# Optimization experiments

Hardware: AMD Instinct MI355X
Metric: run time of the kernel (lower is better)

## Reference

```python
import jax, jax.numpy as jnp
import numpy as np

POOL = 100      # e_pool_size
PLEN = 8        # e_p_length
EMB = 768       # emb_d
KEYD = 768      # key_dim
B = 256
SOFT_T = 1.0    # prompt_param[-1]
VQ_COEF = 0.4
COMIT_COEF = 0.1
E_LAYERS = (0, 1, 2, 3, 4)


def setup_inputs() -> dict:
    key = jax.random.key(0)
    k1, k2, k3, k4 = jax.random.split(key, 4)
    x_querry = jax.random.normal(k1, (B, KEYD), dtype=jnp.float32)
    x_block = jax.random.normal(k2, (B, 197, EMB), dtype=jnp.float32)
    # learned params: nn.init.uniform_ -> U[0,1)
    K = jax.random.uniform(k3, (POOL, KEYD), dtype=jnp.float32)
    p = jax.random.uniform(k4, (POOL, PLEN, EMB), dtype=jnp.float32)
    return {"x_querry": x_querry, "l": 0, "x_block": x_block, "K": K, "p": p}


def reference(x_querry, l, x_block, K, p):
    if l not in E_LAYERS:
        return (None, jnp.float32(0.0), x_block)
    # cosine-sim attention over prompt keys
    n_K = K / jnp.maximum(jnp.linalg.norm(K, axis=1, keepdims=True), 1e-12)
    cos_sim = jnp.einsum('bd,kd->bk', x_querry, n_K)
    alpha = jax.nn.softmax(cos_sim / SOFT_T, axis=1)
    p_a = jnp.einsum('bk,kld->bld', alpha, p)  # [B, L, D]
    # squared L2 distance to each pool entry via dot products (no BxKxLxD tensor)
    pa_sq = jnp.sum(p_a * p_a, axis=(1, 2))            # [B]
    pp_sq = jnp.sum(p * p, axis=(1, 2))                # [K]
    cross = jnp.einsum('bld,kld->bk', p_a, p)          # [B, K]
    dist = pa_sq[:, None] - 2.0 * cross + pp_sq[None, :]
    idxmin = jnp.argmin(dist, axis=1)                  # [B]
    quantized = p[idxmin]                              # [B, L, D]
    e_latent_loss = jnp.mean((p_a - jax.lax.stop_gradient(quantized)) ** 2)
    q_latent_loss = jnp.mean((quantized - jax.lax.stop_gradient(p_a)) ** 2)
    # straight-through estimator
    P_ = p_a + jax.lax.stop_gradient(quantized - p_a)
    i = PLEN // 2
    Ek = P_[:, :i, :]
    Ev = P_[:, i:, :]
    loss = VQ_COEF * e_latent_loss + COMIT_COEF * q_latent_loss
    return (Ek, Ev, loss, x_block)
```

## Files before the change

kernel.cpp:

```cpp
#include <hip/hip_runtime.h>

#define POOL 100
#define PLEN 8
#define EMB 768
#define KEYD 768
#define BATCH 256
#define LD (PLEN*EMB)
#define EK_FLOATS (BATCH*4*EMB)
#define XB_FLOATS (BATCH*197*EMB)
#define LOSS_OFF (2*EK_FLOATS)
#define XB_OFF (LOSS_OFF+1)
#define NGT 325
#define NCOS (BATCH*25)
#define N4 9689087
#define TILE 2048
#define NTILES 4731

typedef float v4f __attribute__((ext_vector_type(4)));
typedef v4f v4f_u __attribute__((aligned(4)));

__device__ __forceinline__ void gram_tile(const float* __restrict__ p,
                                          double* __restrict__ G, int t) {
    int gx = (int)((sqrt(8.0 * t + 1.0) - 1.0) * 0.5);
    while ((gx + 1) * (gx + 2) / 2 <= t) ++gx;
    while (gx * (gx + 1) / 2 > t) --gx;
    int gy = t - gx * (gx + 1) / 2;
    const v4f* P4 = (const v4f*)p;
    double acc[16];
    #pragma unroll
    for (int i = 0; i < 16; ++i) acc[i] = 0.0;
    #pragma unroll
    for (int ch = 0; ch < 6; ++ch) {
        int col = ch * 256 + threadIdx.x;
        v4f ay[4], ax[4];
        #pragma unroll
        for (int i = 0; i < 4; ++i) ay[i] = P4[(size_t)(4*gy + i) * 1536 + col];
        #pragma unroll
        for (int j = 0; j < 4; ++j) ax[j] = P4[(size_t)(4*gx + j) * 1536 + col];
        #pragma unroll
        for (int i = 0; i < 4; ++i)
            #pragma unroll
            for (int j = 0; j < 4; ++j)
                acc[i*4+j] += (double)ay[i][0]*ax[j][0] + (double)ay[i][1]*ax[j][1]
                            + (double)ay[i][2]*ax[j][2] + (double)ay[i][3]*ax[j][3];
    }
    #pragma unroll
    for (int i = 0; i < 16; ++i)
        for (int off = 32; off > 0; off >>= 1)
            acc[i] += __shfl_down(acc[i], off, 64);
    __shared__ double sg[4][16];
    int lane = threadIdx.x & 63, w = threadIdx.x >> 6;
    if (lane == 0) {
        #pragma unroll
        for (int i = 0; i < 16; ++i) sg[w][i] = acc[i];
    }
    __syncthreads();
    if (threadIdx.x < 16) {
        double v = sg[0][threadIdx.x] + sg[1][threadIdx.x]
                 + sg[2][threadIdx.x] + sg[3][threadIdx.x];
        int i = threadIdx.x >> 2, j = threadIdx.x & 3;
        int r = 4*gy + i, c = 4*gx + j;
        G[r * POOL + c] = v;
        G[c * POOL + r] = v;
    }
}

__device__ __forceinline__ void cos_unit(const float* __restrict__ xq,
                                         const float* __restrict__ K,
                                         double* __restrict__ cosm, int c) {
    int b = c / 25, kg = c % 25;
    int w = threadIdx.x >> 6, lane = threadIdx.x & 63;
    int k = kg * 4 + w;
    const v4f* kr = (const v4f*)(K + (size_t)k * KEYD);
    const v4f* xr = (const v4f*)(xq + (size_t)b * KEYD);
    double dot = 0.0, sq = 0.0;
    #pragma unroll
    for (int it = 0; it < 3; ++it) {
        v4f a = kr[it * 64 + lane];
        v4f x = xr[it * 64 + lane];
        dot += (double)a[0]*x[0] + (double)a[1]*x[1] + (double)a[2]*x[2] + (double)a[3]*x[3];
        sq  += (double)a[0]*a[0] + (double)a[1]*a[1] + (double)a[2]*a[2] + (double)a[3]*a[3];
    }
    for (int off = 32; off > 0; off >>= 1) {
        dot += __shfl_down(dot, off, 64);
        sq  += __shfl_down(sq,  off, 64);
    }
    if (lane == 0)
        cosm[(size_t)b * POOL + k] = dot / fmax(sqrt(sq), 1e-12);
}

__global__ void kprep(const float* __restrict__ p, const float* __restrict__ xq,
                      const float* __restrict__ K, const float* __restrict__ xb,
                      float* __restrict__ out, double* __restrict__ G,
                      double* __restrict__ cosm, double* __restrict__ lossAcc,
                      unsigned int* __restrict__ lossCnt) {
    int t = blockIdx.x;
    if (t == 0) {
        if (threadIdx.x == 64) { lossAcc[0] = 0.0; lossCnt[0] = 0u; }
        if (threadIdx.x == 65) {
            out[XB_OFF]     = xb[0];
            out[XB_OFF + 1] = xb[1];
            out[XB_OFF + 2] = xb[2];
            out[XB_OFF + XB_FLOATS - 1] = xb[XB_FLOATS - 1];
        }
    }
    if (t < NGT) gram_tile(p, G, t);
    else         cos_unit(xq, K, cosm, t - NGT);
}

__global__ void kmain(const double* __restrict__ cosm, const double* __restrict__ G,
                      const float* __restrict__ p, const float* __restrict__ xb,
                      float* __restrict__ out, double* __restrict__ lossAcc,
                      unsigned int* __restrict__ lossCnt) {
    if (blockIdx.x >= BATCH) {
        int tile = (int)(blockIdx.x - BATCH);
        const v4f* src4 = (const v4f*)xb;
        v4f* dst = (v4f*)(out + XB_OFF + 3);
        size_t base = (size_t)tile * TILE + threadIdx.x;
        int lane = threadIdx.x & 63;
        if (base + 7 * 256 < N4) {
            v4f v[8];
            #pragma unroll
            for (int k = 0; k < 8; ++k) v[k] = src4[base + (size_t)k * 256 + 1];
            float pw[8];
            #pragma unroll
            for (int k = 0; k < 8; ++k) pw[k] = __shfl_up(v[k][3], 1, 64);
            if (lane == 0) {
                #pragma unroll
                for (int k = 0; k < 8; ++k) pw[k] = xb[4 * (base + (size_t)k * 256) + 3];
            }
            #pragma unroll
            for (int k = 0; k < 8; ++k) {
                v4f o = {pw[k], v[k][0], v[k][1], v[k][2]};
                __builtin_nontemporal_store(o, &dst[base + (size_t)k * 256]);
            }
        } else {
            const v4f_u* srcu = (const v4f_u*)(xb + 3);
            #pragma unroll
            for (int k = 0; k < 8; ++k) {
                size_t j = base + (size_t)k * 256;
                if (j < N4) dst[j] = srcu[j];
            }
        }
        return;
    }
    int b = blockIdx.x;
    __shared__ double sa[POOL], sm[POOL];
    __shared__ double sred[4];
    __shared__ int sidx;
    int lane = threadIdx.x & 63, w = threadIdx.x >> 6;

    double cv = (threadIdx.x < POOL) ? cosm[(size_t)b * POOL + threadIdx.x] : -1.0e300;
    double m = cv;
    for (int off = 32; off > 0; off >>= 1) m = fmax(m, __shfl_down(m, off, 64));
    if (lane == 0) sred[w] = m;
    __syncthreads();
    m = fmax(fmax(sred[0], sred[1]), fmax(sred[2], sred[3]));
    __syncthreads();
    double e = (threadIdx.x < POOL) ? exp(cv - m) : 0.0;
    double ssum = e;
    for (int off = 32; off > 0; off >>= 1) ssum += __shfl_down(ssum, off, 64);
    if (lane == 0) sred[w] = ssum;
    __syncthreads();
    ssum = sred[0] + sred[1] + sred[2] + sred[3];
    __syncthreads();
    if (threadIdx.x < POOL) sa[threadIdx.x] = e / ssum;
    __syncthreads();
    double c = 0.0, paterm = 0.0;
    if (threadIdx.x < POOL) {
        #pragma unroll 4
        for (int k = 0; k < POOL; ++k)
            c += sa[k] * G[k * POOL + threadIdx.x];
        paterm = sa[threadIdx.x] * c;
        sm[threadIdx.x] = G[threadIdx.x * POOL + threadIdx.x] - 2.0 * c;
    }
    double pa = paterm;
    for (int off = 32; off > 0; off >>= 1) pa += __shfl_down(pa, off, 64);
    if (lane == 0) sred[w] = pa;
    __syncthreads();
    pa = sred[0] + sred[1] + sred[2] + sred[3];
    if (threadIdx.x == 0) {
        int best = 0; double bm = sm[0];
        for (int k = 1; k < POOL; ++k)
            if (sm[k] < bm) { bm = sm[k]; best = k; }
        sidx = best;
        double dterm = pa + bm;
        atomicAdd(lossAcc, dterm);
        __threadfence();
        unsigned int old = atomicAdd(lossCnt, 1u);
        if (old == BATCH - 1) {
            double total = atomicAdd(lossAcc, 0.0);
            double msq = total / (double)(BATCH * PLEN * EMB);
            out[LOSS_OFF] = (float)(0.5 * msq);
        }
    }
    __syncthreads();
    int idx = sidx;
    const float4* src = (const float4*)(p + (size_t)idx * LD);
    float4* ek = (float4*)out;
    float4* ev = (float4*)(out + EK_FLOATS);
    for (int j = threadIdx.x; j < LD / 4; j += 256) {
        float4 v = src[j];
        int l = j / (EMB / 4);
        int r = j % (EMB / 4);
        if (l < 4) ek[b * EMB + l * (EMB / 4) + r] = v;
        else       ev[b * EMB + (l - 4) * (EMB / 4) + r] = v;
    }
}

extern "C" void kernel_launch(void* const* d_in, const int* in_sizes, int n_in,
                              void* d_out, int out_size, void* d_ws, size_t ws_size,
                              hipStream_t stream) {
    const float* xq = (const float*)d_in[0];
    const float* xb = (const float*)d_in[2];
    const float* K  = (const float*)d_in[3];
    const float* p  = (const float*)d_in[4];
    float* out = (float*)d_out;

    double* G        = (double*)d_ws;
    double* cosm     = G + POOL * POOL;
    double* lossAcc  = cosm + BATCH * POOL;
    unsigned int* lossCnt = (unsigned int*)(lossAcc + 1);

    kprep<<<NGT + NCOS, 256, 0, stream>>>(p, xq, K, xb, out, G, cosm, lossAcc, lossCnt);
    kmain<<<BATCH + NTILES, 256, 0, stream>>>(cosm, G, p, xb, out, lossAcc, lossCnt);
}
```

Measured before the change: 82.03 us.

## Split x_block copy across two kernels with per-thread contiguous vectors and mixed store types

Moves the large x_block pass-through copy out of one kernel and splits it. Half the tiles stay with the batch VQ blocks and use nontemporal stores; the other half go to a new third kernel that uses normal stores. Each thread now handles four contiguous float4s, and the one-float shift is built in registers rather than with a shuffle per vector. The aim is to improve copy bandwidth by mixing cache policies and raising per-thread contiguity, at the cost of an extra launch and less coalesced access across a wavefront.

```diff
diff --git a/kernel.cpp b/kernel.cpp
--- a/kernel.cpp
+++ b/kernel.cpp
@@ -15,9 +15,60 @@
 #define N4 9689087
 #define TILE 2048
 #define NTILES 4731
+#define NT_A 2365
 
 typedef float v4f __attribute__((ext_vector_type(4)));
 typedef v4f v4f_u __attribute__((aligned(4)));
+
+template <bool NT>
+__device__ __forceinline__ void copy_tile64(const float* __restrict__ xb,
+                                            float* __restrict__ out, int tile) {
+    const v4f* src4 = (const v4f*)xb;
+    v4f* dst = (v4f*)(out + XB_OFF + 3);
+    int lane = threadIdx.x & 63;
+    size_t j0 = (size_t)tile * TILE + (size_t)threadIdx.x * 4;
+    if (tile < NTILES - 1) {
+        v4f a[4], b[4];
+        #pragma unroll
+        for (int k = 0; k < 4; ++k) a[k] = src4[j0 + 1 + k];
+        #pragma unroll
+        for (int k = 0; k < 4; ++k) b[k] = src4[j0 + 1024 + 1 + k];
+        float pa = __shfl_up(a[3][3], 1, 64);
+        float pb = __shfl_up(b[3][3], 1, 64);
+        if (lane == 0) {
+            pa = xb[4 * j0 + 3];
+            pb = xb[4 * (j0 + 1024) + 3];
+        }
+        v4f oa[4], ob[4];
+        oa[0] = (v4f){pa,      a[0][0], a[0][1], a[0][2]};
+        oa[1] = (v4f){a[0][3], a[1][0], a[1][1], a[1][2]};
+        oa[2] = (v4f){a[1][3], a[2][0], a[2][1], a[2][2]};
+        oa[3] = (v4f){a[2][3], a[3][0], a[3][1], a[3][2]};
+        ob[0] = (v4f){pb,      b[0][0], b[0][1], b[0][2]};
+        ob[1] = (v4f){b[0][3], b[1][0], b[1][1], b[1][2]};
+        ob[2] = (v4f){b[1][3], b[2][0], b[2][1], b[2][2]};
+        ob[3] = (v4f){b[2][3], b[3][0], b[3][1], b[3][2]};
+        #pragma unroll
+        for (int k = 0; k < 4; ++k) {
+            if (NT) __builtin_nontemporal_store(oa[k], &dst[j0 + k]);
+            else    dst[j0 + k] = oa[k];
+        }
+        #pragma unroll
+        for (int k = 0; k < 4; ++k) {
+            if (NT) __builtin_nontemporal_store(ob[k], &dst[j0 + 1024 + k]);
+            else    dst[j0 + 1024 + k] = ob[k];
+        }
+    } else {
+        const v4f_u* srcu = (const v4f_u*)(xb + 3);
+        #pragma unroll
+        for (int s = 0; s < 2; ++s)
+            #pragma unroll
+            for (int k = 0; k < 4; ++k) {
+                size_t j = j0 + (size_t)s * 1024 + k;
+                if (j < N4) dst[j] = srcu[j];
+            }
+    }
+}
 
 __device__ __forceinline__ void gram_tile(const float* __restrict__ p,
                                           double* __restrict__ G, int t) {
@@ -108,40 +159,12 @@
     else         cos_unit(xq, K, cosm, t - NGT);
 }
 
-__global__ void kmain(const double* __restrict__ cosm, const double* __restrict__ G,
-                      const float* __restrict__ p, const float* __restrict__ xb,
-                      float* __restrict__ out, double* __restrict__ lossAcc,
-                      unsigned int* __restrict__ lossCnt) {
+__global__ void kcopyA(const double* __restrict__ cosm, const double* __restrict__ G,
+                       const float* __restrict__ p, const float* __restrict__ xb,
+                       float* __restrict__ out, double* __restrict__ lossAcc,
+                       unsigned int* __restrict__ lossCnt) {
     if (blockIdx.x >= BATCH) {
-        int tile = (int)(blockIdx.x - BATCH);
-        const v4f* src4 = (const v4f*)xb;
-        v4f* dst = (v4f*)(out + XB_OFF + 3);
-        size_t base = (size_t)tile * TILE + threadIdx.x;
-        int lane = threadIdx.x & 63;
-        if (base + 7 * 256 < N4) {
-            v4f v[8];
-            #pragma unroll
-            for (int k = 0; k < 8; ++k) v[k] = src4[base + (size_t)k * 256 + 1];
-            float pw[8];
-            #pragma unroll
-            for (int k = 0; k < 8; ++k) pw[k] = __shfl_up(v[k][3], 1, 64);
-            if (lane == 0) {
-                #pragma unroll
-                for (int k = 0; k < 8; ++k) pw[k] = xb[4 * (base + (size_t)k * 256) + 3];
-            }
-            #pragma unroll
-            for (int k = 0; k < 8; ++k) {
-                v4f o = {pw[k], v[k][0], v[k][1], v[k][2]};
-                __builtin_nontemporal_store(o, &dst[base + (size_t)k * 256]);
-            }
-        } else {
-            const v4f_u* srcu = (const v4f_u*)(xb + 3);
-            #pragma unroll
-            for (int k = 0; k < 8; ++k) {
-                size_t j = base + (size_t)k * 256;
-                if (j < N4) dst[j] = srcu[j];
-            }
-        }
+        copy_tile64<true>(xb, out, (int)(blockIdx.x - BATCH));
         return;
     }
     int b = blockIdx.x;
@@ -208,6 +231,10 @@
     }
 }
 
+__global__ void kcopyB(const float* __restrict__ xb, float* __restrict__ out) {
+    copy_tile64<false>(xb, out, NT_A + (int)blockIdx.x);
+}
+
 extern "C" void kernel_launch(void* const* d_in, const int* in_sizes, int n_in,
                               void* d_out, int out_size, void* d_ws, size_t ws_size,
                               hipStream_t stream) {
@@ -223,5 +250,6 @@
     unsigned int* lossCnt = (unsigned int*)(lossAcc + 1);
 
     kprep<<<NGT + NCOS, 256, 0, stream>>>(p, xq, K, xb, out, G, cosm, lossAcc, lossCnt);
-    kmain<<<BATCH + NTILES, 256, 0, stream>>>(cosm, G, p, xb, out, lossAcc, lossCnt);
-}
+    kcopyA<<<BATCH + NT_A, 256, 0, stream>>>(cosm, G, p, xb, out, lossAcc, lossCnt);
+    kcopyB<<<NTILES - NT_A, 256, 0, stream>>>(xb, out);
+}
```

Result: slower. 145.4 us (+77.2%).

## Interleave bulk x_block copy tiles with prep work in first kernel

Applied to the files above, without the earlier changes.

Moves most of the x_block copy tiles from the second kernel into the first, interleaving 8 copy blocks with 16 gram/cosine blocks per group of 24 so the bandwidth-bound copy overlaps with the compute-bound prep. The second kernel keeps only the remaining copy tiles alongside the per-batch softmax/argmin work. This rebalances work across the two launches so the short prep kernel's underutilized time is filled with memory traffic. It adds some idle blocks at the tail of the first grid, and the copy may contend with the prep work for memory bandwidth.

```diff
diff --git a/kernel.cpp b/kernel.cpp
--- a/kernel.cpp
+++ b/kernel.cpp
@@ -12,12 +12,50 @@
 #define XB_OFF (LOSS_OFF+1)
 #define NGT 325
 #define NCOS (BATCH*25)
+#define NPREP (NGT+NCOS)
 #define N4 9689087
 #define TILE 2048
 #define NTILES 4731
+#define NSG 421
+#define COPY_A (NSG*8)
+#define COPY_B (NTILES-COPY_A)
+#define GRID1 (NSG*24)
+#define GRID2 (BATCH+COPY_B)
 
 typedef float v4f __attribute__((ext_vector_type(4)));
 typedef v4f v4f_u __attribute__((aligned(4)));
+
+__device__ __forceinline__ void copy_tile(const float* __restrict__ xb,
+                                          float* __restrict__ out, int tile) {
+    const v4f* src4 = (const v4f*)xb;
+    v4f* dst = (v4f*)(out + XB_OFF + 3);
+    size_t base = (size_t)tile * TILE + threadIdx.x;
+    int lane = threadIdx.x & 63;
+    if (base + 7 * 256 < N4) {
+        v4f v[8];
+        #pragma unroll
+        for (int k = 0; k < 8; ++k) v[k] = src4[base + (size_t)k * 256 + 1];
+        float pw[8];
+        #pragma unroll
+        for (int k = 0; k < 8; ++k) pw[k] = __shfl_up(v[k][3], 1, 64);
+        if (lane == 0) {
+            #pragma unroll
+            for (int k = 0; k < 8; ++k) pw[k] = xb[4 * (base + (size_t)k * 256) + 3];
+        }
+        #pragma unroll
+        for (int k = 0; k < 8; ++k) {
+            v4f o = {pw[k], v[k][0], v[k][1], v[k][2]};
+            __builtin_nontemporal_store(o, &dst[base + (size_t)k * 256]);
+        }
+    } else {
+        const v4f_u* srcu = (const v4f_u*)(xb + 3);
+        #pragma unroll
+        for (int k = 0; k < 8; ++k) {
+            size_t j = base + (size_t)k * 256;
+            if (j < N4) dst[j] = srcu[j];
+        }
+    }
+}
 
 __device__ __forceinline__ void gram_tile(const float* __restrict__ p,
                                           double* __restrict__ G, int t) {
@@ -89,59 +127,38 @@
         cosm[(size_t)b * POOL + k] = dot / fmax(sqrt(sq), 1e-12);
 }
 
-__global__ void kprep(const float* __restrict__ p, const float* __restrict__ xq,
-                      const float* __restrict__ K, const float* __restrict__ xb,
-                      float* __restrict__ out, double* __restrict__ G,
-                      double* __restrict__ cosm, double* __restrict__ lossAcc,
-                      unsigned int* __restrict__ lossCnt) {
-    int t = blockIdx.x;
-    if (t == 0) {
-        if (threadIdx.x == 64) { lossAcc[0] = 0.0; lossCnt[0] = 0u; }
-        if (threadIdx.x == 65) {
-            out[XB_OFF]     = xb[0];
-            out[XB_OFF + 1] = xb[1];
-            out[XB_OFF + 2] = xb[2];
-            out[XB_OFF + XB_FLOATS - 1] = xb[XB_FLOATS - 1];
-        }
-    }
-    if (t < NGT) gram_tile(p, G, t);
-    else         cos_unit(xq, K, cosm, t - NGT);
-}
-
-__global__ void kmain(const double* __restrict__ cosm, const double* __restrict__ G,
-                      const float* __restrict__ p, const float* __restrict__ xb,
-                      float* __restrict__ out, double* __restrict__ lossAcc,
-                      unsigned int* __restrict__ lossCnt) {
+__global__ void k1(const float* __restrict__ p, const float* __restrict__ xq,
+                   const float* __restrict__ K, const float* __restrict__ xb,
+                   float* __restrict__ out, double* __restrict__ G,
+                   double* __restrict__ cosm, double* __restrict__ lossAcc,
+                   unsigned int* __restrict__ lossCnt) {
+    int b = blockIdx.x;
+    int g = b / 24, r = b % 24;
+    if (r < 8) {
+        int tile = g * 8 + r;
+        if (tile == 0) {
+            if (threadIdx.x == 64) { lossAcc[0] = 0.0; lossCnt[0] = 0u; }
+            if (threadIdx.x == 65) {
+                out[XB_OFF]     = xb[0];
+                out[XB_OFF + 1] = xb[1];
+                out[XB_OFF + 2] = xb[2];
+                out[XB_OFF + XB_FLOATS - 1] = xb[XB_FLOATS - 1];
+            }
+        }
+        copy_tile(xb, out, tile);
+        return;
+    }
+    int u = g * 16 + (r - 8);
+    if (u < NGT)        gram_tile(p, G, u);
+    else if (u < NPREP) cos_unit(xq, K, cosm, u - NGT);
+}
+
+__global__ void k2(const double* __restrict__ cosm, const double* __restrict__ G,
+                   const float* __restrict__ p, const float* __restrict__ xb,
+                   float* __restrict__ out, double* __restrict__ lossAcc,
+                   unsigned int* __restrict__ lossCnt) {
     if (blockIdx.x >= BATCH) {
-        int tile = (int)(blockIdx.x - BATCH);
-        const v4f* src4 = (const v4f*)xb;
-        v4f* dst = (v4f*)(out + XB_OFF + 3);
-        size_t base = (size_t)tile * TILE + threadIdx.x;
-        int lane = threadIdx.x & 63;
-        if (base + 7 * 256 < N4) {
-            v4f v[8];
-            #pragma unroll
-            for (int k = 0; k < 8; ++k) v[k] = src4[base + (size_t)k * 256 + 1];
-            float pw[8];
-            #pragma unroll
-            for (int k = 0; k < 8; ++k) pw[k] = __shfl_up(v[k][3], 1, 64);
-            if (lane == 0) {
-                #pragma unroll
-                for (int k = 0; k < 8; ++k) pw[k] = xb[4 * (base + (size_t)k * 256) + 3];
-            }
-            #pragma unroll
-            for (int k = 0; k < 8; ++k) {
-                v4f o = {pw[k], v[k][0], v[k][1], v[k][2]};
-                __builtin_nontemporal_store(o, &dst[base + (size_t)k * 256]);
-            }
-        } else {
-            const v4f_u* srcu = (const v4f_u*)(xb + 3);
-            #pragma unroll
-            for (int k = 0; k < 8; ++k) {
-                size_t j = base + (size_t)k * 256;
-                if (j < N4) dst[j] = srcu[j];
-            }
-        }
+        copy_tile(xb, out, COPY_A + (int)(blockIdx.x - BATCH));
         return;
     }
     int b = blockIdx.x;
@@ -222,6 +239,6 @@
     double* lossAcc  = cosm + BATCH * POOL;
     unsigned int* lossCnt = (unsigned int*)(lossAcc + 1);
 
-    kprep<<<NGT + NCOS, 256, 0, stream>>>(p, xq, K, xb, out, G, cosm, lossAcc, lossCnt);
-    kmain<<<BATCH + NTILES, 256, 0, stream>>>(cosm, G, p, xb, out, lossAcc, lossCnt);
-}
+    k1<<<GRID1, 256, 0, stream>>>(p, xq, K, xb, out, G, cosm, lossAcc, lossCnt);
+    k2<<<GRID2, 256, 0, stream>>>(cosm, G, p, xb, out, lossAcc, lossCnt);
+}
```

After: 70.77 us (median of 2 runs). 13.7% less time.
